# Kernel tuning notes

Hardware: AMD Instinct MI355X
Metric: run time of the kernel (lower is better)

Reference implementation:

```python
import jax, jax.numpy as jnp
import numpy as np

B, T, H, C = 64, 512, 1024, 21  # batch, seq_len, hidden_size, num_labels


def setup_inputs() -> dict:
    key = jax.random.key(0)
    ks = jax.random.split(key, 7)
    hidden_states = jax.random.normal(ks[0], (B, T, H), dtype=jnp.float32)
    lengths = jax.random.randint(ks[1], (B,), 1, T + 1)  # at least 1 valid token
    attention_mask = jnp.arange(T)[None, :] < lengths[:, None]  # [B,T] bool, contiguous prefix
    labels = jax.random.randint(ks[2], (B, T), 0, C)
    # classifier params (nn.Linear(H, C))
    W = jax.random.normal(ks[3], (H, C), dtype=jnp.float32) * 0.02
    b = jnp.zeros((C,), dtype=jnp.float32)
    # CRF params (torchcrf init: uniform(-0.1, 0.1))
    transitions = jax.random.uniform(ks[4], (C, C), minval=-0.1, maxval=0.1, dtype=jnp.float32)
    start_transitions = jax.random.uniform(ks[5], (C,), minval=-0.1, maxval=0.1, dtype=jnp.float32)
    end_transitions = jax.random.uniform(ks[6], (C,), minval=-0.1, maxval=0.1, dtype=jnp.float32)
    return {
        "hidden_states": hidden_states,
        "W": W,
        "b": b,
        "transitions": transitions,
        "start_transitions": start_transitions,
        "end_transitions": end_transitions,
        "attention_mask": attention_mask,
        "labels": labels,
    }


def _crf_nll(emissions, tags, mask, transitions, start_transitions, end_transitions):
    """Mean negative log-likelihood of torchcrf CRF(batch_first=True, reduction='mean')."""
    maskf = mask.astype(emissions.dtype)
    # ---- numerator: score of the gold tag path ----
    em_tag = jnp.take_along_axis(emissions, tags[..., None], axis=2)[..., 0]  # [B,T]
    trans_score = transitions[tags[:, :-1], tags[:, 1:]]                      # [B,T-1]
    num = (start_transitions[tags[:, 0]] + em_tag[:, 0]
           + jnp.sum((trans_score + em_tag[:, 1:]) * maskf[:, 1:], axis=1))
    last_idx = jnp.sum(mask.astype(jnp.int32), axis=1) - 1                    # [B]
    last_tag = jnp.take_along_axis(tags, last_idx[:, None], axis=1)[:, 0]
    num = num + end_transitions[last_tag]
    # ---- denominator: forward algorithm (log partition) ----
    alpha0 = start_transitions[None, :] + emissions[:, 0]                     # [B,C]

    def step(alpha, xs):
        em_t, m_t = xs  # [B,C], [B]
        nxt = jax.nn.logsumexp(alpha[:, :, None] + transitions[None, :, :] + em_t[:, None, :], axis=1)
        return jnp.where(m_t[:, None], nxt, alpha), None

    xs = (jnp.swapaxes(emissions[:, 1:], 0, 1), jnp.swapaxes(mask[:, 1:], 0, 1))
    alphaT, _ = jax.lax.scan(step, alpha0, xs)
    logZ = jax.nn.logsumexp(alphaT + end_transitions[None, :], axis=1)        # [B]
    llh = num - logZ
    return -jnp.mean(llh)


def reference(hidden_states, W, b, transitions, start_transitions, end_transitions,
              attention_mask, labels):
    # dropout is identity at inference; emissions = Linear(hidden)
    emissions = jnp.einsum('bth,hc->btc', hidden_states, W) + b              # [B,T,C]
    # mask logic from the module: attention_mask & (labels != -100); mask[:,0] = True
    mask = attention_mask & (labels != -100)
    mask = mask.at[:, 0].set(True)
    loss = _crf_nll(emissions, labels, mask, transitions, start_transitions, end_transitions)
    return emissions, loss
```

## Files before the change

### kernel.cpp

```cpp
#include <hip/hip_runtime.h>

#define BB 64
#define TT 512
#define HH 1024
#define CC 21
#define NROWS (BB*TT)

typedef __attribute__((ext_vector_type(8)))  short  short8;
typedef __attribute__((ext_vector_type(16))) float  float16;

__global__ __launch_bounds__(256) void wprep(const float* __restrict__ W,
                                             unsigned short* __restrict__ wpad) {
  int idx = blockIdx.x * 256 + threadIdx.x;
  int n = idx >> 10, k = idx & 1023;
  float v = (n < CC) ? W[k * CC + n] : 0.f;
  unsigned b = __float_as_uint(v);
  float lo = v - __uint_as_float(b & 0xFFFF0000u);
  wpad[idx]         = (unsigned short)(b >> 16);
  wpad[32768 + idx] = (unsigned short)(__float_as_uint(lo) >> 16);
}

__global__ __launch_bounds__(64) void emis_mfma(const float* __restrict__ hs,
                                                const unsigned short* __restrict__ wpad,
                                                const float* __restrict__ bias,
                                                float* __restrict__ out) {
  const int lane = threadIdx.x;
  const int m    = lane & 31;
  const int half = lane >> 5;
  const int row0 = blockIdx.x * 32;

  if (blockIdx.x == 0 && lane == 0) out[(size_t)NROWS * CC] = 0.f;

  const float4* arow =
      reinterpret_cast<const float4*>(hs + (size_t)(row0 + m) * HH) + half * 2;
  const unsigned short* whi = wpad + m * 1024 + half * 8;
  const unsigned short* wlo = whi + 32768;

  float16 acc;
#pragma unroll
  for (int i = 0; i < 16; ++i) acc[i] = 0.f;

  float4 xa[8], xb[8];
#pragma unroll
  for (int i = 0; i < 8; ++i) { xa[i] = arow[i * 4]; xb[i] = arow[i * 4 + 1]; }
  short8 bhq[4], blq[4];
#pragma unroll
  for (int i = 0; i < 4; ++i) {
    bhq[i] = *reinterpret_cast<const short8*>(whi + i * 16);
    blq[i] = *reinterpret_cast<const short8*>(wlo + i * 16);
  }

#pragma unroll 8
  for (int kb = 0; kb < 64; ++kb) {
    const int s8 = kb & 7, s4 = kb & 3;
    float4 a0 = xa[s8], a1 = xb[s8];
    int kn = kb + 8; if (kn > 63) kn = 63;
    xa[s8] = arow[kn * 4];
    xb[s8] = arow[kn * 4 + 1];
    short8 bh = bhq[s4], bl = blq[s4];
    int kw = kb + 4; if (kw > 63) kw = 63;
    bhq[s4] = *reinterpret_cast<const short8*>(whi + kw * 16);
    blq[s4] = *reinterpret_cast<const short8*>(wlo + kw * 16);

    float af[8] = {a0.x, a0.y, a0.z, a0.w, a1.x, a1.y, a1.z, a1.w};
    short8 ah, al;
#pragma unroll
    for (int j = 0; j < 8; ++j) {
      unsigned b = __float_as_uint(af[j]);
      ah[j] = (short)(b >> 16);
      float lo = af[j] - __uint_as_float(b & 0xFFFF0000u);
      al[j] = (short)(__float_as_uint(lo) >> 16);
    }
    acc = __builtin_amdgcn_mfma_f32_32x32x16_bf16(ah, bh, acc, 0, 0, 0);
    acc = __builtin_amdgcn_mfma_f32_32x32x16_bf16(ah, bl, acc, 0, 0, 0);
    acc = __builtin_amdgcn_mfma_f32_32x32x16_bf16(al, bh, acc, 0, 0, 0);
  }

  float bv = (m < CC) ? bias[m] : 0.f;
#pragma unroll
  for (int r = 0; r < 16; ++r) {
    int row = (r & 3) + 8 * (r >> 2) + 4 * half;
    if (m < CC) out[(size_t)(row0 + row) * CC + m] = acc[r] + bv;
  }
}

__global__ __launch_bounds__(128) void crf_kernel(const float* __restrict__ em,
                                                  const float* __restrict__ trans,
                                                  const float* __restrict__ startT,
                                                  const float* __restrict__ endT,
                                                  const int* __restrict__ att,
                                                  const int* __restrict__ labels,
                                                  float* __restrict__ loss) {
  const int b    = blockIdx.x;
  const int tid  = threadIdx.x;
  const int wave = tid >> 6;
  const int lane = tid & 63;
  __shared__ float sh_num;
  __shared__ int   sh_len;

  const float L2E = 1.4426950408889634f;
  const float LN2 = 0.6931471805599453f;

  if (wave == 1) {
    int cnt = 0;
    for (int t = lane; t < TT; t += 64) {
      bool m = (t == 0) || ((att[b * TT + t] != 0) && (labels[b * TT + t] != -100));
      cnt += m ? 1 : 0;
    }
#pragma unroll
    for (int off = 32; off >= 1; off >>= 1) cnt += __shfl_down(cnt, off);
    cnt = __shfl(cnt, 0);

    float s = 0.f;
    for (int t = lane + 1; t < TT; t += 64) {
      bool m = (att[b * TT + t] != 0) && (labels[b * TT + t] != -100);
      if (m) {
        int tp = labels[b * TT + t - 1], tc = labels[b * TT + t];
        s += trans[tp * CC + tc] + em[((size_t)b * TT + t) * CC + tc];
      }
    }
#pragma unroll
    for (int off = 32; off >= 1; off >>= 1) s += __shfl_down(s, off);
    if (lane == 0) {
      int tag0 = labels[b * TT];
      int lastTag = labels[b * TT + cnt - 1];
      s += startT[tag0] + em[((size_t)b * TT) * CC + tag0] + endT[lastTag];
      sh_num = s;
      sh_len = cnt;
    }
  }

  const int j = lane < CC ? lane : CC - 1;
  float E[CC], F[CC];
  float f = 0.f, g = 0.f;
  if (wave == 0) {
#pragma unroll
    for (int i = 0; i < CC; ++i) {
      E[i] = __builtin_amdgcn_exp2f(trans[i * CC + j] * L2E);
      F[i] = __builtin_amdgcn_exp2f(trans[j * CC + i] * L2E);
    }
    f = __builtin_amdgcn_exp2f((startT[j] + em[((size_t)b * TT) * CC + j]) * L2E);
    g = __builtin_amdgcn_exp2f(endT[j] * L2E);
  }
  __syncthreads();
  if (wave != 0) return;

  const int len = sh_len;
  const int L  = len - 1;
  const int mF = (L + 1) >> 1;
  const int mB = L - mF;
  int kf = 0, kg = 0;

  float sf[CC];
#pragma unroll
  for (int i = 0; i < CC; ++i)
    sf[i] = __int_as_float(__builtin_amdgcn_readlane(__float_as_int(f), i));

  const float* emB = em + (size_t)b * TT * CC;

  float rf[4], rb[4];
#pragma unroll
  for (int u = 0; u < 4; ++u) {
    int tf = 1 + u; if (tf > TT - 1) tf = TT - 1;
    rf[u] = emB[(size_t)tf * CC + j];
    int tb = len - 1 - u; if (tb < 0) tb = 0;
    rb[u] = emB[(size_t)tb * CC + j];
  }

  int it = 0;
  while (it < mF) {
#pragma unroll
    for (int u = 0; u < 4; ++u) {
      const int i2 = it + u;
      if (i2 < mF) {
        float pm = __builtin_amdgcn_exp2f(rf[u] * L2E);
        int tp = 1 + i2 + 4; if (tp > TT - 1) tp = TT - 1;
        rf[u] = emB[(size_t)tp * CC + j];
        int ef = (__float_as_int(sf[0]) >> 23) & 255;
        kf += ef - 127;
        float pms = pm * __int_as_float((254 - ef) << 23);
        float c0 = 0.f, c1 = 0.f, c2 = 0.f;
#pragma unroll
        for (int i = 0; i < CC; i += 3) c0 = fmaf(sf[i], E[i], c0);
#pragma unroll
        for (int i = 1; i < CC; i += 3) c1 = fmaf(sf[i], E[i], c1);
#pragma unroll
        for (int i = 2; i < CC; i += 3) c2 = fmaf(sf[i], E[i], c2);
        f = ((c0 + c1) + c2) * pms;
#pragma unroll
        for (int i = 0; i < CC; ++i)
          sf[i] = __int_as_float(__builtin_amdgcn_readlane(__float_as_int(f), i));
      }
      if (i2 < mB) {
        float pm = __builtin_amdgcn_exp2f(rb[u] * L2E);
        int tb = len - 1 - i2 - 4; if (tb < 0) tb = 0;
        rb[u] = emB[(size_t)tb * CC + j];
        float h = pm * g;
        float sh_[CC];
#pragma unroll
        for (int i = 0; i < CC; ++i)
          sh_[i] = __int_as_float(__builtin_amdgcn_readlane(__float_as_int(h), i));
        int eg = (__float_as_int(sh_[0]) >> 23) & 255;
        kg += eg - 127;
        float sB = __int_as_float((254 - eg) << 23);
        float d0 = 0.f, d1 = 0.f, d2 = 0.f;
#pragma unroll
        for (int i = 0; i < CC; i += 3) d0 = fmaf(sh_[i], F[i], d0);
#pragma unroll
        for (int i = 1; i < CC; i += 3) d1 = fmaf(sh_[i], F[i], d1);
#pragma unroll
        for (int i = 2; i < CC; i += 3) d2 = fmaf(sh_[i], F[i], d2);
        g = ((d0 + d1) + d2) * sB;
      }
    }
    it += 4;
  }

  float v = (lane < CC) ? f * g : 0.f;
#pragma unroll
  for (int off = 32; off >= 1; off >>= 1) v += __shfl_xor(v, off);
  if (lane == 0) {
    float logZ = (float)(kf + kg) * LN2 + LN2 * __builtin_amdgcn_logf(v);
    atomicAdd(loss, -(sh_num - logZ) * (1.0f / 64.0f));
  }
}

extern "C" void kernel_launch(void* const* d_in, const int* in_sizes, int n_in,
                              void* d_out, int out_size, void* d_ws, size_t ws_size,
                              hipStream_t stream) {
  const float* hs     = (const float*)d_in[0];
  const float* W      = (const float*)d_in[1];
  const float* bias   = (const float*)d_in[2];
  const float* trans  = (const float*)d_in[3];
  const float* startT = (const float*)d_in[4];
  const float* endT   = (const float*)d_in[5];
  const int*   att    = (const int*)d_in[6];
  const int*   labels = (const int*)d_in[7];
  float* out = (float*)d_out;
  unsigned short* wpad = (unsigned short*)d_ws;

  wprep<<<dim3(128), dim3(256), 0, stream>>>(W, wpad);
  emis_mfma<<<dim3(1024), dim3(64), 0, stream>>>(hs, wpad, bias, out);
  crf_kernel<<<dim3(64), dim3(128), 0, stream>>>(out, trans, startT, endT, att,
                                                 labels, out + (size_t)NROWS * CC);
}
```

Baseline: 289.2 us.

## Stage hidden-state tiles through double-buffered LDS and pre-swizzle W into MFMA fragments

The emission GEMM now loads hidden-state rows as coalesced 64-column chunks (16 lanes per row), writes them into a padded, double-buffered shared-memory tile, and reads MFMA A operands from LDS. Before, each lane streamed its own row with strided float4 loads. W is pre-packed in MFMA fragment order so each lane fetches its B operand with one contiguous short8 load. The CRF kernel's arrays are unrolled into named scalars via macros so they stay in registers, and both waves now compute the exp tables. This adds LDS traffic, a per-chunk store/load round trip and register pressure from the prefetch buffer.

```diff
diff --git a/kernel.cpp b/kernel.cpp
--- a/kernel.cpp
+++ b/kernel.cpp
@@ -5,84 +5,104 @@
 #define HH 1024
 #define CC 21
 #define NROWS (BB*TT)
+#define TSTR 68
 
 typedef __attribute__((ext_vector_type(8)))  short  short8;
 typedef __attribute__((ext_vector_type(16))) float  float16;
 
 __global__ __launch_bounds__(256) void wprep(const float* __restrict__ W,
-                                             unsigned short* __restrict__ wpad) {
+                                             unsigned short* __restrict__ wf) {
   int idx = blockIdx.x * 256 + threadIdx.x;
-  int n = idx >> 10, k = idx & 1023;
+  int q = idx >> 9;
+  int l = (idx >> 3) & 63;
+  int j = idx & 7;
+  int k = q * 16 + (l >> 5) * 8 + j;
+  int n = l & 31;
   float v = (n < CC) ? W[k * CC + n] : 0.f;
   unsigned b = __float_as_uint(v);
   float lo = v - __uint_as_float(b & 0xFFFF0000u);
-  wpad[idx]         = (unsigned short)(b >> 16);
-  wpad[32768 + idx] = (unsigned short)(__float_as_uint(lo) >> 16);
+  wf[idx]         = (unsigned short)(b >> 16);
+  wf[32768 + idx] = (unsigned short)(__float_as_uint(lo) >> 16);
 }
 
 __global__ __launch_bounds__(64) void emis_mfma(const float* __restrict__ hs,
-                                                const unsigned short* __restrict__ wpad,
+                                                const unsigned short* __restrict__ wfrag,
                                                 const float* __restrict__ bias,
                                                 float* __restrict__ out) {
+  __shared__ float tile[2][32 * TSTR];
   const int lane = threadIdx.x;
-  const int m    = lane & 31;
-  const int half = lane >> 5;
+  const int m = lane & 31, h = lane >> 5;
   const int row0 = blockIdx.x * 32;
+  const int r_ = lane >> 4;
+  const int sg = lane & 15;
 
   if (blockIdx.x == 0 && lane == 0) out[(size_t)NROWS * CC] = 0.f;
 
-  const float4* arow =
-      reinterpret_cast<const float4*>(hs + (size_t)(row0 + m) * HH) + half * 2;
-  const unsigned short* whi = wpad + m * 1024 + half * 8;
-  const unsigned short* wlo = whi + 32768;
-
   float16 acc;
 #pragma unroll
   for (int i = 0; i < 16; ++i) acc[i] = 0.f;
 
-  float4 xa[8], xb[8];
-#pragma unroll
-  for (int i = 0; i < 8; ++i) { xa[i] = arow[i * 4]; xb[i] = arow[i * 4 + 1]; }
-  short8 bhq[4], blq[4];
-#pragma unroll
-  for (int i = 0; i < 4; ++i) {
-    bhq[i] = *reinterpret_cast<const short8*>(whi + i * 16);
-    blq[i] = *reinterpret_cast<const short8*>(wlo + i * 16);
-  }
-
-#pragma unroll 8
-  for (int kb = 0; kb < 64; ++kb) {
-    const int s8 = kb & 7, s4 = kb & 3;
-    float4 a0 = xa[s8], a1 = xb[s8];
-    int kn = kb + 8; if (kn > 63) kn = 63;
-    xa[s8] = arow[kn * 4];
-    xb[s8] = arow[kn * 4 + 1];
-    short8 bh = bhq[s4], bl = blq[s4];
-    int kw = kb + 4; if (kw > 63) kw = 63;
-    bhq[s4] = *reinterpret_cast<const short8*>(whi + kw * 16);
-    blq[s4] = *reinterpret_cast<const short8*>(wlo + kw * 16);
-
-    float af[8] = {a0.x, a0.y, a0.z, a0.w, a1.x, a1.y, a1.z, a1.w};
-    short8 ah, al;
-#pragma unroll
-    for (int j = 0; j < 8; ++j) {
-      unsigned b = __float_as_uint(af[j]);
-      ah[j] = (short)(b >> 16);
-      float lo = af[j] - __uint_as_float(b & 0xFFFF0000u);
-      al[j] = (short)(__float_as_uint(lo) >> 16);
-    }
-    acc = __builtin_amdgcn_mfma_f32_32x32x16_bf16(ah, bh, acc, 0, 0, 0);
-    acc = __builtin_amdgcn_mfma_f32_32x32x16_bf16(ah, bl, acc, 0, 0, 0);
-    acc = __builtin_amdgcn_mfma_f32_32x32x16_bf16(al, bh, acc, 0, 0, 0);
+  float4 buf[8];
+#pragma unroll
+  for (int i = 0; i < 8; ++i)
+    buf[i] = *reinterpret_cast<const float4*>(
+        hs + (size_t)(row0 + 4 * i + r_) * HH + sg * 4);
+#pragma unroll
+  for (int i = 0; i < 8; ++i)
+    *reinterpret_cast<float4*>(&tile[0][(4 * i + r_) * TSTR + sg * 4]) = buf[i];
+
+  for (int c = 0; c < 16; ++c) {
+    const int pb = c & 1;
+    if (c < 15) {
+#pragma unroll
+      for (int i = 0; i < 8; ++i)
+        buf[i] = *reinterpret_cast<const float4*>(
+            hs + (size_t)(row0 + 4 * i + r_) * HH + (c + 1) * 64 + sg * 4);
+    }
+#pragma unroll
+    for (int s = 0; s < 4; ++s) {
+      const float* ap = &tile[pb][m * TSTR + s * 16 + h * 8];
+      float4 a0 = *reinterpret_cast<const float4*>(ap);
+      float4 a1 = *reinterpret_cast<const float4*>(ap + 4);
+      float af[8] = {a0.x, a0.y, a0.z, a0.w, a1.x, a1.y, a1.z, a1.w};
+      short8 ah, al;
+#pragma unroll
+      for (int jj = 0; jj < 8; ++jj) {
+        unsigned b = __float_as_uint(af[jj]);
+        ah[jj] = (short)(b >> 16);
+        float lo = af[jj] - __uint_as_float(b & 0xFFFF0000u);
+        al[jj] = (short)(__float_as_uint(lo) >> 16);
+      }
+      const int q = c * 4 + s;
+      short8 bh = *reinterpret_cast<const short8*>(wfrag + q * 512 + lane * 8);
+      short8 bl = *reinterpret_cast<const short8*>(wfrag + 32768 + q * 512 + lane * 8);
+      acc = __builtin_amdgcn_mfma_f32_32x32x16_bf16(ah, bh, acc, 0, 0, 0);
+      acc = __builtin_amdgcn_mfma_f32_32x32x16_bf16(ah, bl, acc, 0, 0, 0);
+      acc = __builtin_amdgcn_mfma_f32_32x32x16_bf16(al, bh, acc, 0, 0, 0);
+    }
+    if (c < 15) {
+#pragma unroll
+      for (int i = 0; i < 8; ++i)
+        *reinterpret_cast<float4*>(&tile[pb ^ 1][(4 * i + r_) * TSTR + sg * 4]) = buf[i];
+    }
   }
 
   float bv = (m < CC) ? bias[m] : 0.f;
 #pragma unroll
   for (int r = 0; r < 16; ++r) {
-    int row = (r & 3) + 8 * (r >> 2) + 4 * half;
+    int row = (r & 3) + 8 * (r >> 2) + 4 * h;
     if (m < CC) out[(size_t)(row0 + row) * CC + m] = acc[r] + bv;
   }
 }
+
+#define REP21(X) X(0) X(1) X(2) X(3) X(4) X(5) X(6) X(7) X(8) X(9) X(10) \
+                 X(11) X(12) X(13) X(14) X(15) X(16) X(17) X(18) X(19) X(20)
+
+#define DE(i)  float E##i = __builtin_amdgcn_exp2f(trans[(i) * CC + j] * L2E);
+#define DF(i)  float F##i = __builtin_amdgcn_exp2f(trans[j * CC + (i)] * L2E);
+#define DSF(i) float sf##i = __int_as_float(__builtin_amdgcn_readlane(__float_as_int(f), i));
+#define ASF(i) sf##i = __int_as_float(__builtin_amdgcn_readlane(__float_as_int(f), i));
+#define DSH(i) float sh##i = __int_as_float(__builtin_amdgcn_readlane(__float_as_int(h_), i));
 
 __global__ __launch_bounds__(128) void crf_kernel(const float* __restrict__ em,
                                                   const float* __restrict__ trans,
@@ -104,8 +124,8 @@
   if (wave == 1) {
     int cnt = 0;
     for (int t = lane; t < TT; t += 64) {
-      bool m = (t == 0) || ((att[b * TT + t] != 0) && (labels[b * TT + t] != -100));
-      cnt += m ? 1 : 0;
+      bool mm = (t == 0) || ((att[b * TT + t] != 0) && (labels[b * TT + t] != -100));
+      cnt += mm ? 1 : 0;
     }
 #pragma unroll
     for (int off = 32; off >= 1; off >>= 1) cnt += __shfl_down(cnt, off);
@@ -113,8 +133,8 @@
 
     float s = 0.f;
     for (int t = lane + 1; t < TT; t += 64) {
-      bool m = (att[b * TT + t] != 0) && (labels[b * TT + t] != -100);
-      if (m) {
+      bool mm = (att[b * TT + t] != 0) && (labels[b * TT + t] != -100);
+      if (mm) {
         int tp = labels[b * TT + t - 1], tc = labels[b * TT + t];
         s += trans[tp * CC + tc] + em[((size_t)b * TT + t) * CC + tc];
       }
@@ -131,17 +151,10 @@
   }
 
   const int j = lane < CC ? lane : CC - 1;
-  float E[CC], F[CC];
-  float f = 0.f, g = 0.f;
-  if (wave == 0) {
-#pragma unroll
-    for (int i = 0; i < CC; ++i) {
-      E[i] = __builtin_amdgcn_exp2f(trans[i * CC + j] * L2E);
-      F[i] = __builtin_amdgcn_exp2f(trans[j * CC + i] * L2E);
-    }
-    f = __builtin_amdgcn_exp2f((startT[j] + em[((size_t)b * TT) * CC + j]) * L2E);
-    g = __builtin_amdgcn_exp2f(endT[j] * L2E);
-  }
+  REP21(DE)
+  REP21(DF)
+  float f = __builtin_amdgcn_exp2f((startT[j] + em[((size_t)b * TT) * CC + j]) * L2E);
+  float g = __builtin_amdgcn_exp2f(endT[j] * L2E);
   __syncthreads();
   if (wave != 0) return;
 
@@ -151,10 +164,7 @@
   const int mB = L - mF;
   int kf = 0, kg = 0;
 
-  float sf[CC];
-#pragma unroll
-  for (int i = 0; i < CC; ++i)
-    sf[i] = __int_as_float(__builtin_amdgcn_readlane(__float_as_int(f), i));
+  REP21(DSF)
 
   const float* emB = em + (size_t)b * TT * CC;
 
@@ -176,40 +186,35 @@
         float pm = __builtin_amdgcn_exp2f(rf[u] * L2E);
         int tp = 1 + i2 + 4; if (tp > TT - 1) tp = TT - 1;
         rf[u] = emB[(size_t)tp * CC + j];
-        int ef = (__float_as_int(sf[0]) >> 23) & 255;
+        int ef = (__float_as_int(sf0) >> 23) & 255;
         kf += ef - 127;
         float pms = pm * __int_as_float((254 - ef) << 23);
-        float c0 = 0.f, c1 = 0.f, c2 = 0.f;
-#pragma unroll
-        for (int i = 0; i < CC; i += 3) c0 = fmaf(sf[i], E[i], c0);
-#pragma unroll
-        for (int i = 1; i < CC; i += 3) c1 = fmaf(sf[i], E[i], c1);
-#pragma unroll
-        for (int i = 2; i < CC; i += 3) c2 = fmaf(sf[i], E[i], c2);
+        float c0 = sf0 * E0, c1 = sf1 * E1, c2 = sf2 * E2;
+        c0 = fmaf(sf3,  E3,  c0); c1 = fmaf(sf4,  E4,  c1); c2 = fmaf(sf5,  E5,  c2);
+        c0 = fmaf(sf6,  E6,  c0); c1 = fmaf(sf7,  E7,  c1); c2 = fmaf(sf8,  E8,  c2);
+        c0 = fmaf(sf9,  E9,  c0); c1 = fmaf(sf10, E10, c1); c2 = fmaf(sf11, E11, c2);
+        c0 = fmaf(sf12, E12, c0); c1 = fmaf(sf13, E13, c1); c2 = fmaf(sf14, E14, c2);
+        c0 = fmaf(sf15, E15, c0); c1 = fmaf(sf16, E16, c1); c2 = fmaf(sf17, E17, c2);
+        c0 = fmaf(sf18, E18, c0); c1 = fmaf(sf19, E19, c1); c2 = fmaf(sf20, E20, c2);
         f = ((c0 + c1) + c2) * pms;
-#pragma unroll
-        for (int i = 0; i < CC; ++i)
-          sf[i] = __int_as_float(__builtin_amdgcn_readlane(__float_as_int(f), i));
+        REP21(ASF)
       }
       if (i2 < mB) {
         float pm = __builtin_amdgcn_exp2f(rb[u] * L2E);
         int tb = len - 1 - i2 - 4; if (tb < 0) tb = 0;
         rb[u] = emB[(size_t)tb * CC + j];
-        float h = pm * g;
-        float sh_[CC];
-#pragma unroll
-        for (int i = 0; i < CC; ++i)
-          sh_[i] = __int_as_float(__builtin_amdgcn_readlane(__float_as_int(h), i));
-        int eg = (__float_as_int(sh_[0]) >> 23) & 255;
+        float h_ = pm * g;
+        REP21(DSH)
+        int eg = (__float_as_int(sh0) >> 23) & 255;
         kg += eg - 127;
         float sB = __int_as_float((254 - eg) << 23);
-        float d0 = 0.f, d1 = 0.f, d2 = 0.f;
-#pragma unroll
-        for (int i = 0; i < CC; i += 3) d0 = fmaf(sh_[i], F[i], d0);
-#pragma unroll
-        for (int i = 1; i < CC; i += 3) d1 = fmaf(sh_[i], F[i], d1);
-#pragma unroll
-        for (int i = 2; i < CC; i += 3) d2 = fmaf(sh_[i], F[i], d2);
+        float d0 = sh0 * F0, d1 = sh1 * F1, d2 = sh2 * F2;
+        d0 = fmaf(sh3,  F3,  d0); d1 = fmaf(sh4,  F4,  d1); d2 = fmaf(sh5,  F5,  d2);
+        d0 = fmaf(sh6,  F6,  d0); d1 = fmaf(sh7,  F7,  d1); d2 = fmaf(sh8,  F8,  d2);
+        d0 = fmaf(sh9,  F9,  d0); d1 = fmaf(sh10, F10, d1); d2 = fmaf(sh11, F11, d2);
+        d0 = fmaf(sh12, F12, d0); d1 = fmaf(sh13, F13, d1); d2 = fmaf(sh14, F14, d2);
+        d0 = fmaf(sh15, F15, d0); d1 = fmaf(sh16, F16, d1); d2 = fmaf(sh17, F17, d2);
+        d0 = fmaf(sh18, F18, d0); d1 = fmaf(sh19, F19, d1); d2 = fmaf(sh20, F20, d2);
         g = ((d0 + d1) + d2) * sB;
       }
     }
@@ -237,10 +242,10 @@
   const int*   att    = (const int*)d_in[6];
   const int*   labels = (const int*)d_in[7];
   float* out = (float*)d_out;
-  unsigned short* wpad = (unsigned short*)d_ws;
-
-  wprep<<<dim3(128), dim3(256), 0, stream>>>(W, wpad);
-  emis_mfma<<<dim3(1024), dim3(64), 0, stream>>>(hs, wpad, bias, out);
+  unsigned short* wfrag = (unsigned short*)d_ws;
+
+  wprep<<<dim3(128), dim3(256), 0, stream>>>(W, wfrag);
+  emis_mfma<<<dim3(1024), dim3(64), 0, stream>>>(hs, wfrag, bias, out);
   crf_kernel<<<dim3(64), dim3(128), 0, stream>>>(out, trans, startT, endT, att,
                                                  labels, out + (size_t)NROWS * CC);
 }
```

After: 347.3 us. 20.1% more time.
